# Kernel optimization log

Hardware: AMD Instinct MI355X
Metric: run time of the kernel (lower is better)

Reference implementation:

```python
import jax, jax.numpy as jnp
import numpy as np

B, H, W, C = 32, 56, 56, 192
HEADS = 6
WS = 7            # window size
SS = 3            # shift size
N = WS * WS       # tokens per window (49)
HID = 4 * C
EPS = 1e-5


def _rel_index():
    coords = np.stack(np.meshgrid(np.arange(WS), np.arange(WS), indexing='ij')).reshape(2, -1)
    rel = (coords[:, :, None] - coords[:, None, :]).transpose(1, 2, 0)
    rel[:, :, 0] += WS - 1
    rel[:, :, 1] += WS - 1
    rel[:, :, 0] *= 2 * WS - 1
    return rel.sum(-1)  # [N, N] int


def _attn_mask():
    # shift mask, identical to the torch construction; static -> numpy
    m = np.zeros((H, W))
    cnt = 0
    for hs in (slice(0, -WS), slice(-WS, -SS), slice(-SS, None)):
        for ws in (slice(0, -WS), slice(-WS, -SS), slice(-SS, None)):
            m[hs, ws] = cnt
            cnt += 1
    mw = m.reshape(H // WS, WS, W // WS, WS).transpose(0, 2, 1, 3).reshape(-1, N)  # [nW, N]
    diff = mw[:, None, :] - mw[:, :, None]
    return np.where(diff != 0, -100.0, 0.0).astype(np.float32)  # [nW, N, N]

REL_IDX = jnp.asarray(_rel_index())
ATTN_MASK = jnp.asarray(_attn_mask())


def setup_inputs() -> dict:
    key = jax.random.key(0)
    ks = jax.random.split(key, 16)
    s = 0.02
    return {
        'x': jax.random.normal(ks[0], (B, H, W, C), jnp.float32),
        'norm1_g': jnp.ones((C,), jnp.float32),
        'norm1_b': jnp.zeros((C,), jnp.float32),
        'qkv_w': jax.random.normal(ks[1], (C, 3 * C), jnp.float32) * s,
        'qkv_b': jnp.zeros((3 * C,), jnp.float32),
        'proj_w': jax.random.normal(ks[2], (C, C), jnp.float32) * s,
        'proj_b': jnp.zeros((C,), jnp.float32),
        'bias_table': jax.random.normal(ks[3], ((2 * WS - 1) ** 2, HEADS), jnp.float32) * s,
        'norm2_g': jnp.ones((C,), jnp.float32),
        'norm2_b': jnp.zeros((C,), jnp.float32),
        'fc1_w': jax.random.normal(ks[4], (C, HID), jnp.float32) * s,
        'fc1_b': jnp.zeros((HID,), jnp.float32),
        'fc2_w': jax.random.normal(ks[5], (HID, C), jnp.float32) * s,
        'fc2_b': jnp.zeros((C,), jnp.float32),
    }


def _ln(x, g, b):
    mu = jnp.mean(x, -1, keepdims=True)
    var = jnp.var(x, -1, keepdims=True)
    return (x - mu) * jax.lax.rsqrt(var + EPS) * g + b


def _partition(x):
    # [B,H,W,C] -> [B*nW, N, C]
    return x.reshape(B, H // WS, WS, W // WS, WS, C).transpose(0, 1, 3, 2, 4, 5).reshape(-1, N, C)


def _reverse(w):
    # [B*nW, N, C] -> [B,H,W,C]
    return w.reshape(B, H // WS, W // WS, WS, WS, C).transpose(0, 1, 3, 2, 4, 5).reshape(B, H, W, C)


def reference(x, norm1_g, norm1_b, qkv_w, qkv_b, proj_w, proj_b, bias_table,
              norm2_g, norm2_b, fc1_w, fc1_b, fc2_w, fc2_b):
    hd = C // HEADS
    scale = hd ** -0.5
    sc = x
    h = _ln(x, norm1_g, norm1_b)
    h = jnp.roll(h, (-SS, -SS), (1, 2))
    xw = _partition(h)                                  # [B_, N, C]
    B_ = xw.shape[0]
    qkv = (xw @ qkv_w + qkv_b).reshape(B_, N, 3, HEADS, hd).transpose(2, 0, 3, 1, 4)
    q, k, v = qkv[0], qkv[1], qkv[2]                    # [B_, H, N, hd]
    attn = jnp.einsum('bhnd,bhmd->bhnm', q * scale, k)  # [B_, H, N, N]
    bias = bias_table[REL_IDX.reshape(-1)].reshape(N, N, HEADS).transpose(2, 0, 1)
    attn = attn + bias[None]
    nW = (H // WS) * (W // WS)
    attn = attn.reshape(B, nW, HEADS, N, N) + ATTN_MASK[None, :, None]
    attn = jax.nn.softmax(attn.reshape(-1, HEADS, N, N), axis=-1)
    out = jnp.einsum('bhnm,bhmd->bhnd', attn, v).transpose(0, 2, 1, 3).reshape(B_, N, C)
    out = out @ proj_w + proj_b
    h = _reverse(out)
    h = jnp.roll(h, (SS, SS), (1, 2))
    y = sc + h
    m = _ln(y, norm2_g, norm2_b)
    mlp = jax.nn.gelu(m @ fc1_w + fc1_b, approximate=False) @ fc2_w + fc2_b
    return y + mlp
```

## Files before the change

### kernel.cpp

```cpp
#include <hip/hip_runtime.h>
#include <hip/hip_bf16.h>

typedef __hip_bfloat16 bf16;
typedef float f32x4 __attribute__((ext_vector_type(4)));
typedef short bf16x8 __attribute__((ext_vector_type(8)));
typedef short short4v __attribute__((ext_vector_type(4)));
typedef unsigned int u32;

#define NTOK 100352
#define CC 192
#define HIDN 768

__device__ __forceinline__ float b2f(unsigned short u) {
    union { unsigned int u32v; float f; } x; x.u32v = ((unsigned int)u) << 16; return x.f;
}
__device__ __forceinline__ unsigned short f2b(float f) {
    union { float f; unsigned int u; } x; x.f = f;
    unsigned int r = x.u + 0x7FFF + ((x.u >> 16) & 1);
    return (unsigned short)(r >> 16);
}

typedef __attribute__((address_space(1))) const unsigned char gas_u8;
typedef __attribute__((address_space(3))) unsigned char las_u8;
__device__ __forceinline__ void gload_lds16(const void* g, void* l) {
    __builtin_amdgcn_global_load_lds((gas_u8*)g, (las_u8*)l, 16, 0, 0);
}

__global__ void transpose_k(const float* __restrict__ src, bf16* __restrict__ dst,
                            int R, int C, int Cpad) {
    int idx = blockIdx.x * 256 + threadIdx.x;
    if (idx >= R * Cpad) return;
    int c = idx / R, r = idx % R;
    dst[idx] = (c < C) ? __float2bfloat16(src[(size_t)r * C + c]) : __float2bfloat16(0.0f);
}

__global__ void bm_k(const float* __restrict__ btab, float* __restrict__ bm) {
    int idx = blockIdx.x * 256 + threadIdx.x;
    if (idx >= 98304) return;
    int reg = idx & 3, lane = (idx >> 2) & 63, tile = (idx >> 8) & 15;
    int rest = idx >> 12, h = rest % 6, cls = rest / 6;
    int mt = tile >> 2, nt = tile & 3;
    int kk = mt * 16 + (lane >> 4) * 4 + reg;
    int q  = nt * 16 + (lane & 15);
    float v;
    if (kk >= 49 || q >= 49) v = -1e9f;
    else {
        int i1 = q / 7, j1 = q % 7, i2 = kk / 7, j2 = kk % 7;
        v = btab[((i1 - i2 + 6) * 13 + (j1 - j2 + 6)) * 6 + h];
        int hb7 = cls >> 1, wb7 = cls & 1;
        int r1 = (hb7 ? (i1 < 4 ? 1 : 2) : 0) * 3 + (wb7 ? (j1 < 4 ? 1 : 2) : 0);
        int r2 = (hb7 ? (i2 < 4 ? 1 : 2) : 0) * 3 + (wb7 ? (j2 < 4 ? 1 : 2) : 0);
        if (r1 != r2) v -= 100.0f;
    }
    bm[idx] = v;
}

template<bool GATHER>
__global__ __launch_bounds__(256) void ln_k(const float* __restrict__ src,
                                            const float* __restrict__ gamma,
                                            const float* __restrict__ beta,
                                            bf16* __restrict__ dst) {
    int wave = threadIdx.x >> 6, lane = threadIdx.x & 63;
    int t = blockIdx.x * 4 + wave;
    size_t srow;
    if (GATHER) {
        int w = t / 49, n = t % 49;
        int b = w >> 6, wl = w & 63, hb = wl >> 3, wb = wl & 7;
        int i = n / 7, j = n % 7;
        int sh = hb * 7 + i + 3; if (sh >= 56) sh -= 56;
        int sw = wb * 7 + j + 3; if (sw >= 56) sw -= 56;
        srow = ((size_t)(b * 56 + sh) * 56 + sw) * CC;
    } else {
        srow = (size_t)t * CC;
    }
    float v[4];
    int c = lane * 4;
    float sum = 0.f, sq = 0.f;
    if (lane < 48) {
        f32x4 d = *(const f32x4*)(src + srow + c);
        #pragma unroll
        for (int q = 0; q < 4; ++q) { v[q] = d[q]; sum += v[q]; sq += v[q] * v[q]; }
    }
    #pragma unroll
    for (int off = 1; off < 64; off <<= 1) { sum += __shfl_xor(sum, off); sq += __shfl_xor(sq, off); }
    float mu = sum * (1.0f / 192.0f);
    float var = sq * (1.0f / 192.0f) - mu * mu;
    float rstd = rsqrtf(var + 1e-5f);
    if (lane < 48) {
        f32x4 gg = *(const f32x4*)(gamma + c);
        f32x4 bb = *(const f32x4*)(beta + c);
        short4v o;
        #pragma unroll
        for (int q = 0; q < 4; ++q) {
            float val = (v[q] - mu) * rstd * gg[q] + bb[q];
            o[q] = (short)f2b(val);
        }
        *(short4v*)(dst + (size_t)t * CC + c) = o;
    }
}

template<int EPI, int WIDE>
__global__ __launch_bounds__(256) void gemm_t(
    const bf16* __restrict__ X, const bf16* __restrict__ WT,
    const float* __restrict__ bias, int K, int N, int NR,
    bf16* __restrict__ outb, float* __restrict__ outf,
    const float* __restrict__ xres, const float* __restrict__ yin, int mbase)
{
    constexpr int BN = WIDE ? 128 : 64;
    constexpr int NF = WIDE ? 4 : 2;
    constexpr int NBJ = WIDE ? 4 : 2;
    __shared__ bf16 As[2][128 * 64];
    __shared__ bf16 Bs[2][BN * 64];
    const int tid = threadIdx.x;
    const int w = tid >> 6, lane = tid & 63;
    const int w0 = w & 1, w1 = w >> 1;
    const int nOff = WIDE ? w0 * 64 : w0 * 32;

    const u32 nwg = gridDim.x * gridDim.y;
    u32 bid = blockIdx.y * gridDim.x + blockIdx.x;
    if ((nwg & 7) == 0) bid = (bid & 7) * (nwg >> 3) + (bid >> 3);
    const int tn0 = (bid % gridDim.x) * BN;
    const int tm0 = (bid / gridDim.x) * 128;

    const int r16 = lane & 15, g8 = (lane >> 4) * 8;

    const bf16* gA[4];
    const bf16* gB[NBJ];
    #pragma unroll
    for (int j = 0; j < 4; ++j) {
        int c = (w * 4 + j) * 64 + lane;
        int l = c ^ ((c >> 3) & 7);
        gA[j] = X + (size_t)(tm0 + (c >> 3)) * K + (l & 7) * 8;
    }
    #pragma unroll
    for (int j = 0; j < NBJ; ++j) {
        int c = (w * NBJ + j) * 64 + lane;
        int l = c ^ ((c >> 3) & 7);
        gB[j] = WT + (size_t)(tn0 + (c >> 3)) * K + (l & 7) * 8;
    }

    auto stage = [&](int buf, int kk) {
        #pragma unroll
        for (int j = 0; j < 4; ++j)
            gload_lds16(gA[j] + kk, (char*)&As[buf][0] + (size_t)(w * 4 + j) * 1024);
        #pragma unroll
        for (int j = 0; j < NBJ; ++j)
            gload_lds16(gB[j] + kk, (char*)&Bs[buf][0] + (size_t)(w * NBJ + j) * 1024);
    };

    f32x4 acc[4][NF] = {};
    const int nt = K >> 6;
    stage(0, 0);
    __syncthreads();
    for (int t = 0; t < nt; ++t) {
        int buf = t & 1;
        if (t + 1 < nt) stage(buf ^ 1, (t + 1) << 6);
        const char* ab = (const char*)&As[buf][0];
        const char* bb_ = (const char*)&Bs[buf][0];
        #pragma unroll
        for (int k32 = 0; k32 < 2; ++k32) {
            int kcolb = k32 * 64 + g8 * 2;
            bf16x8 a[4], b[NF];
            #pragma unroll
            for (int m = 0; m < 4; ++m) {
                int row = w1 * 64 + m * 16 + r16;
                int byte = row * 128 + kcolb;
                a[m] = *(const bf16x8*)(ab + (byte ^ ((row & 7) << 4)));
            }
            #pragma unroll
            for (int n = 0; n < NF; ++n) {
                int row = nOff + n * 16 + r16;
                int byte = row * 128 + kcolb;
                b[n] = *(const bf16x8*)(bb_ + (byte ^ ((row & 7) << 4)));
            }
            #pragma unroll
            for (int m = 0; m < 4; ++m)
                #pragma unroll
                for (int n = 0; n < NF; ++n)
                    acc[m][n] = __builtin_amdgcn_mfma_f32_16x16x32_bf16(a[m], b[n], acc[m][n], 0, 0, 0);
        }
        __syncthreads();
    }

    #pragma unroll
    for (int n = 0; n < NF; ++n) {
        int col = tn0 + nOff + n * 16 + r16;
        if (col >= NR) continue;
        float bv = bias[col];
        #pragma unroll
        for (int m = 0; m < 4; ++m) {
            #pragma unroll
            for (int r = 0; r < 4; ++r) {
                int mm = tm0 + w1 * 64 + m * 16 + (lane >> 4) * 4 + r;
                float val = acc[m][n][r] + bv;
                if (EPI == 0) {
                    outb[(size_t)mm * NR + col] = __float2bfloat16(val);
                } else if (EPI == 1) {
                    int gm = mbase + mm;
                    int ww = gm / 49, nn = gm % 49;
                    int b_ = ww >> 6, wl = ww & 63, hb = wl >> 3, wb = wl & 7;
                    int i = nn / 7, j = nn % 7;
                    int oh = hb * 7 + i + 3; if (oh >= 56) oh -= 56;
                    int ow = wb * 7 + j + 3; if (ow >= 56) ow -= 56;
                    size_t dst = ((size_t)(b_ * 56 + oh) * 56 + ow) * CC + col;
                    outf[dst] = xres[dst] + val;
                } else if (EPI == 2) {
                    float gv = 0.5f * val * (1.0f + erff(val * 0.70710678118f));
                    outb[(size_t)mm * NR + col] = __float2bfloat16(gv);
                } else if (EPI == 3) {
                    outf[(size_t)mm * NR + col] = val + yin[(size_t)mm * NR + col];
                } else {
                    outb[((size_t)(col >> 5) * NTOK + mm) * 32 + (col & 31)] = __float2bfloat16(val);
                }
            }
        }
    }
}

__global__ __launch_bounds__(384) void attn_m(const bf16* __restrict__ qkv,
                                              const float* __restrict__ bm,
                                              bf16* __restrict__ out)
{
    __shared__ char Pl[6][8192];
    __shared__ char Vt[6][4096];
    const int w = blockIdx.x;
    const int h = threadIdx.x >> 6, l = threadIdx.x & 63;
    const int w49 = w * 49;
    const int wl = w & 63;
    const int cls = (((wl >> 3) == 7) ? 2 : 0) + (((wl & 7) == 7) ? 1 : 0);
    const int hi8 = (l >> 4) * 8, lo = l & 15;

    {
        const bf16* vbase = qkv + ((size_t)(12 + h) * NTOK + w49) * 32;
        #pragma unroll
        for (int it = 0; it < 4; ++it) {
            int c = it * 64 + l;
            int kk = c >> 2, off = (c & 3) * 8;
            bf16x8 v = {};
            if (c < 196) v = *(const bf16x8*)(vbase + kk * 32 + off);
            #pragma unroll
            for (int j = 0; j < 8; ++j) {
                int d = off + j;
                int byte = (d * 128 + kk * 2) ^ ((d & 7) << 4);
                *(bf16*)(&Vt[h][0] + byte) = ((const bf16*)&v)[j];
            }
        }
    }

    const bf16* qb = qkv + ((size_t)h * NTOK + w49) * 32 + hi8;
    const bf16* kb = qkv + ((size_t)(6 + h) * NTOK + w49) * 32 + hi8;
    bf16x8 af[4], bf_[4];
    #pragma unroll
    for (int mt = 0; mt < 4; ++mt) af[mt] = *(const bf16x8*)(kb + (size_t)(mt * 16 + lo) * 32);
    #pragma unroll
    for (int ntt = 0; ntt < 4; ++ntt) bf_[ntt] = *(const bf16x8*)(qb + (size_t)(ntt * 16 + lo) * 32);
    f32x4 acc[4][4] = {};
    #pragma unroll
    for (int mt = 0; mt < 4; ++mt)
        #pragma unroll
        for (int ntt = 0; ntt < 4; ++ntt)
            acc[mt][ntt] = __builtin_amdgcn_mfma_f32_16x16x32_bf16(af[mt], bf_[ntt], acc[mt][ntt], 0, 0, 0);

    const float scale = 0.17677669529663689f;
    const float* bmb = bm + ((size_t)(cls * 6 + h) << 4) * 256;
    #pragma unroll
    for (int mt = 0; mt < 4; ++mt)
        #pragma unroll
        for (int ntt = 0; ntt < 4; ++ntt) {
            f32x4 bmv = *(const f32x4*)(bmb + (mt * 4 + ntt) * 256 + l * 4);
            #pragma unroll
            for (int r = 0; r < 4; ++r) acc[mt][ntt][r] = acc[mt][ntt][r] * scale + bmv[r];
        }

    float inv[4], mx[4];
    #pragma unroll
    for (int ntt = 0; ntt < 4; ++ntt) {
        float m_ = -1e30f;
        #pragma unroll
        for (int mt = 0; mt < 4; ++mt)
            #pragma unroll
            for (int r = 0; r < 4; ++r) m_ = fmaxf(m_, acc[mt][ntt][r]);
        m_ = fmaxf(m_, __shfl_xor(m_, 16));
        m_ = fmaxf(m_, __shfl_xor(m_, 32));
        mx[ntt] = m_;
    }
    #pragma unroll
    for (int ntt = 0; ntt < 4; ++ntt) {
        float s_ = 0.f;
        #pragma unroll
        for (int mt = 0; mt < 4; ++mt)
            #pragma unroll
            for (int r = 0; r < 4; ++r) {
                float e = __expf(acc[mt][ntt][r] - mx[ntt]);
                acc[mt][ntt][r] = e;
                s_ += e;
            }
        s_ += __shfl_xor(s_, 16);
        s_ += __shfl_xor(s_, 32);
        inv[ntt] = 1.0f / s_;
    }

    #pragma unroll
    for (int mt = 0; mt < 4; ++mt)
        #pragma unroll
        for (int ntt = 0; ntt < 4; ++ntt)
            #pragma unroll
            for (int rp = 0; rp < 4; rp += 2) {
                u32 pk = (u32)f2b(acc[mt][ntt][rp]) | ((u32)f2b(acc[mt][ntt][rp + 1]) << 16);
                int kk = mt * 16 + (l >> 4) * 4 + rp;
                int q  = ntt * 16 + lo;
                int byte = (q * 128 + kk * 2) ^ ((q & 7) << 4);
                *(u32*)(&Pl[h][0] + byte) = pk;
            }

    f32x4 o[4][2] = {};
    #pragma unroll
    for (int ks = 0; ks < 2; ++ks) {
        int kb_ = (ks * 32 + hi8) * 2;
        bf16x8 pa[4], vb[2];
        #pragma unroll
        for (int qt = 0; qt < 4; ++qt) {
            int row = qt * 16 + lo;
            pa[qt] = *(const bf16x8*)(&Pl[h][0] + ((row * 128 + kb_) ^ ((row & 7) << 4)));
        }
        #pragma unroll
        for (int dt = 0; dt < 2; ++dt) {
            int row = dt * 16 + lo;
            vb[dt] = *(const bf16x8*)(&Vt[h][0] + ((row * 128 + kb_) ^ ((row & 7) << 4)));
        }
        #pragma unroll
        for (int qt = 0; qt < 4; ++qt)
            #pragma unroll
            for (int dt = 0; dt < 2; ++dt)
                o[qt][dt] = __builtin_amdgcn_mfma_f32_16x16x32_bf16(pa[qt], vb[dt], o[qt][dt], 0, 0, 0);
    }

    #pragma unroll
    for (int qt = 0; qt < 4; ++qt)
        #pragma unroll
        for (int r = 0; r < 4; ++r) {
            int qrow = (l >> 4) * 4 + r;
            float iv = __shfl(inv[qt], qrow);
            int q = qt * 16 + qrow;
            if (q < 49) {
                size_t ob = (size_t)(w49 + q) * CC + h * 32 + lo;
                out[ob]      = __float2bfloat16(o[qt][0][r] * iv);
                out[ob + 16] = __float2bfloat16(o[qt][1][r] * iv);
            }
        }
}

extern "C" void kernel_launch(void* const* d_in, const int* in_sizes, int n_in,
                              void* d_out, int out_size, void* d_ws, size_t ws_size,
                              hipStream_t stream) {
    const float* x      = (const float*)d_in[0];
    const float* n1g    = (const float*)d_in[1];
    const float* n1b    = (const float*)d_in[2];
    const float* qkv_w  = (const float*)d_in[3];
    const float* qkv_b  = (const float*)d_in[4];
    const float* proj_w = (const float*)d_in[5];
    const float* proj_b = (const float*)d_in[6];
    const float* btab   = (const float*)d_in[7];
    const float* n2g    = (const float*)d_in[8];
    const float* n2b    = (const float*)d_in[9];
    const float* fc1_w  = (const float*)d_in[10];
    const float* fc1_b  = (const float*)d_in[11];
    const float* fc2_w  = (const float*)d_in[12];
    const float* fc2_b  = (const float*)d_in[13];

    char* ws = (char*)d_ws;
    const size_t XW_OFF  = 0;
    const size_t QKV_OFF = 38535168;
    const size_t ATT_OFF = 154140672;
    const size_t WT_OFF  = 192675840;
    const size_t BM_OFF  = 193585152;
    if (ws_size < 193978368ull) return;

    bf16* xw   = (bf16*)(ws + XW_OFF);
    bf16* mbuf = (bf16*)(ws + XW_OFF);
    bf16* qkvb = (bf16*)(ws + QKV_OFF);
    bf16* attb = (bf16*)(ws + ATT_OFF);
    bf16* hidb = (bf16*)(ws + QKV_OFF);
    float* yf  = (float*)d_out;
    bf16* wt   = (bf16*)(ws + WT_OFF);
    float* bmt = (float*)(ws + BM_OFF);
    bf16* qkv_wT  = wt;
    bf16* proj_wT = wt + 122880;
    bf16* fc1_wT  = wt + 159744;
    bf16* fc2_wT  = wt + 307200;

    transpose_k<<<dim3(480), 256, 0, stream>>>(qkv_w, qkv_wT, 192, 576, 640);
    transpose_k<<<dim3(144), 256, 0, stream>>>(proj_w, proj_wT, 192, 192, 192);
    transpose_k<<<dim3(576), 256, 0, stream>>>(fc1_w, fc1_wT, 192, 768, 768);
    transpose_k<<<dim3(576), 256, 0, stream>>>(fc2_w, fc2_wT, 768, 192, 192);
    bm_k<<<dim3(384), 256, 0, stream>>>(btab, bmt);

    ln_k<true><<<NTOK / 4, 256, 0, stream>>>(x, n1g, n1b, xw);

    gemm_t<4, 1><<<dim3(5, 784), 256, 0, stream>>>(
        xw, qkv_wT, qkv_b, 192, 640, 576, qkvb, nullptr, nullptr, nullptr, 0);
    attn_m<<<dim3(2048), 384, 0, stream>>>(qkvb, bmt, attb);
    gemm_t<1, 0><<<dim3(3, 784), 256, 0, stream>>>(
        attb, proj_wT, proj_b, 192, 192, 192, nullptr, yf, x, nullptr, 0);

    ln_k<false><<<NTOK / 4, 256, 0, stream>>>(yf, n2g, n2b, mbuf);

    gemm_t<2, 1><<<dim3(6, 784), 256, 0, stream>>>(
        mbuf, fc1_wT, fc1_b, 192, 768, 768, hidb, nullptr, nullptr, nullptr, 0);
    gemm_t<3, 0><<<dim3(3, 784), 256, 0, stream>>>(
        hidb, fc2_wT, fc2_b, 768, 192, 192, nullptr, yf, nullptr, yf, 0);
}
```

Measured before the change: 404.9 us.

## Load GEMM weights directly to registers, swap MFMA operands for vectorized epilogue, tanh GELU

The GEMM kernel stops staging the weight tile through LDS and loads weight fragments straight from global memory (L2-resident) into registers each k-step. MFMA operands are swapped so each lane holds four consecutive output columns, which allows 4-wide vector stores and residual loads in the epilogue. Exact erf GELU is replaced by a tanh approximation built on exp. The bid remap is also made unconditional. This cuts LDS traffic and store instruction count, but adds per-iteration global loads with latency not hidden by the double buffer, and changes GELU numerics.

```diff
diff --git a/kernel.cpp b/kernel.cpp
--- a/kernel.cpp
+++ b/kernel.cpp
@@ -18,6 +18,13 @@
     union { float f; unsigned int u; } x; x.f = f;
     unsigned int r = x.u + 0x7FFF + ((x.u >> 16) & 1);
     return (unsigned short)(r >> 16);
+}
+__device__ __forceinline__ float gelu_f(float x) {
+    float x3 = x * x * x;
+    float y2 = 1.5957691216f * (x + 0.044715f * x3);
+    float e = __expf(y2);
+    float th = 1.0f - 2.0f / (e + 1.0f);
+    return 0.5f * x * (1.0f + th);
 }
 
 typedef __attribute__((address_space(1))) const unsigned char gas_u8;
@@ -108,9 +115,7 @@
 {
     constexpr int BN = WIDE ? 128 : 64;
     constexpr int NF = WIDE ? 4 : 2;
-    constexpr int NBJ = WIDE ? 4 : 2;
     __shared__ bf16 As[2][128 * 64];
-    __shared__ bf16 Bs[2][BN * 64];
     const int tid = threadIdx.x;
     const int w = tid >> 6, lane = tid & 63;
     const int w0 = w & 1, w1 = w >> 1;
@@ -118,100 +123,111 @@
 
     const u32 nwg = gridDim.x * gridDim.y;
     u32 bid = blockIdx.y * gridDim.x + blockIdx.x;
-    if ((nwg & 7) == 0) bid = (bid & 7) * (nwg >> 3) + (bid >> 3);
+    bid = (bid & 7) * (nwg >> 3) + (bid >> 3);
     const int tn0 = (bid % gridDim.x) * BN;
     const int tm0 = (bid / gridDim.x) * 128;
 
     const int r16 = lane & 15, g8 = (lane >> 4) * 8;
 
     const bf16* gA[4];
-    const bf16* gB[NBJ];
     #pragma unroll
     for (int j = 0; j < 4; ++j) {
         int c = (w * 4 + j) * 64 + lane;
         int l = c ^ ((c >> 3) & 7);
         gA[j] = X + (size_t)(tm0 + (c >> 3)) * K + (l & 7) * 8;
     }
-    #pragma unroll
-    for (int j = 0; j < NBJ; ++j) {
-        int c = (w * NBJ + j) * 64 + lane;
-        int l = c ^ ((c >> 3) & 7);
-        gB[j] = WT + (size_t)(tn0 + (c >> 3)) * K + (l & 7) * 8;
-    }
-
     auto stage = [&](int buf, int kk) {
         #pragma unroll
         for (int j = 0; j < 4; ++j)
             gload_lds16(gA[j] + kk, (char*)&As[buf][0] + (size_t)(w * 4 + j) * 1024);
-        #pragma unroll
-        for (int j = 0; j < NBJ; ++j)
-            gload_lds16(gB[j] + kk, (char*)&Bs[buf][0] + (size_t)(w * NBJ + j) * 1024);
     };
 
+    const bf16* gW[NF];
+    #pragma unroll
+    for (int n = 0; n < NF; ++n)
+        gW[n] = WT + (size_t)(tn0 + nOff + n * 16 + r16) * K + g8;
+
     f32x4 acc[4][NF] = {};
-    const int nt = K >> 6;
+    const int ntile = K >> 6;
     stage(0, 0);
     __syncthreads();
-    for (int t = 0; t < nt; ++t) {
+    for (int t = 0; t < ntile; ++t) {
         int buf = t & 1;
-        if (t + 1 < nt) stage(buf ^ 1, (t + 1) << 6);
+        if (t + 1 < ntile) stage(buf ^ 1, (t + 1) << 6);
         const char* ab = (const char*)&As[buf][0];
-        const char* bb_ = (const char*)&Bs[buf][0];
         #pragma unroll
         for (int k32 = 0; k32 < 2; ++k32) {
+            int kg = (t << 6) + k32 * 32;
             int kcolb = k32 * 64 + g8 * 2;
-            bf16x8 a[4], b[NF];
+            bf16x8 xf[4], wf[NF];
             #pragma unroll
             for (int m = 0; m < 4; ++m) {
                 int row = w1 * 64 + m * 16 + r16;
                 int byte = row * 128 + kcolb;
-                a[m] = *(const bf16x8*)(ab + (byte ^ ((row & 7) << 4)));
-            }
-            #pragma unroll
-            for (int n = 0; n < NF; ++n) {
-                int row = nOff + n * 16 + r16;
-                int byte = row * 128 + kcolb;
-                b[n] = *(const bf16x8*)(bb_ + (byte ^ ((row & 7) << 4)));
-            }
+                xf[m] = *(const bf16x8*)(ab + (byte ^ ((row & 7) << 4)));
+            }
+            #pragma unroll
+            for (int n = 0; n < NF; ++n)
+                wf[n] = *(const bf16x8*)(gW[n] + kg);
             #pragma unroll
             for (int m = 0; m < 4; ++m)
                 #pragma unroll
                 for (int n = 0; n < NF; ++n)
-                    acc[m][n] = __builtin_amdgcn_mfma_f32_16x16x32_bf16(a[m], b[n], acc[m][n], 0, 0, 0);
+                    acc[m][n] = __builtin_amdgcn_mfma_f32_16x16x32_bf16(wf[n], xf[m], acc[m][n], 0, 0, 0);
         }
         __syncthreads();
     }
 
-    #pragma unroll
-    for (int n = 0; n < NF; ++n) {
-        int col = tn0 + nOff + n * 16 + r16;
-        if (col >= NR) continue;
-        float bv = bias[col];
-        #pragma unroll
-        for (int m = 0; m < 4; ++m) {
-            #pragma unroll
-            for (int r = 0; r < 4; ++r) {
-                int mm = tm0 + w1 * 64 + m * 16 + (lane >> 4) * 4 + r;
-                float val = acc[m][n][r] + bv;
-                if (EPI == 0) {
-                    outb[(size_t)mm * NR + col] = __float2bfloat16(val);
-                } else if (EPI == 1) {
-                    int gm = mbase + mm;
-                    int ww = gm / 49, nn = gm % 49;
-                    int b_ = ww >> 6, wl = ww & 63, hb = wl >> 3, wb = wl & 7;
-                    int i = nn / 7, j = nn % 7;
-                    int oh = hb * 7 + i + 3; if (oh >= 56) oh -= 56;
-                    int ow = wb * 7 + j + 3; if (ow >= 56) ow -= 56;
-                    size_t dst = ((size_t)(b_ * 56 + oh) * 56 + ow) * CC + col;
-                    outf[dst] = xres[dst] + val;
-                } else if (EPI == 2) {
-                    float gv = 0.5f * val * (1.0f + erff(val * 0.70710678118f));
-                    outb[(size_t)mm * NR + col] = __float2bfloat16(gv);
-                } else if (EPI == 3) {
-                    outf[(size_t)mm * NR + col] = val + yin[(size_t)mm * NR + col];
-                } else {
-                    outb[((size_t)(col >> 5) * NTOK + mm) * 32 + (col & 31)] = __float2bfloat16(val);
-                }
+    const int q4 = (lane >> 4) * 4;
+    #pragma unroll
+    for (int mt = 0; mt < 4; ++mt) {
+        int mm = tm0 + w1 * 64 + mt * 16 + r16;
+        size_t rowbase;
+        if (EPI == 1) {
+            int gm = mbase + mm;
+            int ww = gm / 49, nn = gm % 49;
+            int b_ = ww >> 6, wl = ww & 63, hb = wl >> 3, wb = wl & 7;
+            int i = nn / 7, j = nn % 7;
+            int oh = hb * 7 + i + 3; if (oh >= 56) oh -= 56;
+            int ow = wb * 7 + j + 3; if (ow >= 56) ow -= 56;
+            rowbase = ((size_t)(b_ * 56 + oh) * 56 + ow) * CC;
+        } else {
+            rowbase = (size_t)mm * NR;
+        }
+        #pragma unroll
+        for (int nt = 0; nt < NF; ++nt) {
+            int col = tn0 + nOff + nt * 16 + q4;
+            if (col >= NR) continue;
+            f32x4 bv = *(const f32x4*)(bias + col);
+            f32x4 v;
+            #pragma unroll
+            for (int r = 0; r < 4; ++r) v[r] = acc[mt][nt][r] + bv[r];
+            if (EPI == 0) {
+                short4v o;
+                #pragma unroll
+                for (int r = 0; r < 4; ++r) o[r] = (short)f2b(v[r]);
+                *(short4v*)(outb + rowbase + col) = o;
+            } else if (EPI == 1) {
+                f32x4 xr = *(const f32x4*)(xres + rowbase + col);
+                #pragma unroll
+                for (int r = 0; r < 4; ++r) v[r] += xr[r];
+                *(f32x4*)(outf + rowbase + col) = v;
+            } else if (EPI == 2) {
+                short4v o;
+                #pragma unroll
+                for (int r = 0; r < 4; ++r) o[r] = (short)f2b(gelu_f(v[r]));
+                *(short4v*)(outb + rowbase + col) = o;
+            } else if (EPI == 3) {
+                f32x4 yv = *(const f32x4*)(yin + rowbase + col);
+                #pragma unroll
+                for (int r = 0; r < 4; ++r) v[r] += yv[r];
+                *(f32x4*)(outf + rowbase + col) = v;
+            } else {
+                size_t ob = ((size_t)(col >> 5) * NTOK + mm) * 32 + (col & 31);
+                short4v o;
+                #pragma unroll
+                for (int r = 0; r < 4; ++r) o[r] = (short)f2b(v[r]);
+                *(short4v*)(outb + ob) = o;
             }
         }
     }
```

Result: slower. 483.9 us (+19.5%).
